# Optimization experiments

Measured on AMD Instinct MI355X. Metric: run time of the kernel, lower is better.

Reference implementation:

```python
import jax, jax.numpy as jnp
import numpy as np

HEADS = 16
KEY_SIZE = 64
SIZE_PER_HEAD = 64
OUT_DIM = HEADS * SIZE_PER_HEAD  # 1024
BIG = 1e10
B, LQ, LK = 2, 2048, 2048


def setup_inputs() -> dict:
    key = jax.random.key(0)
    ks = jax.random.split(key, 8)
    q = jax.random.normal(ks[0], (B, LQ, OUT_DIM), dtype=jnp.float32)
    k = jax.random.normal(ks[1], (B, LK, OUT_DIM), dtype=jnp.float32)
    v = jax.random.normal(ks[2], (B, LK, OUT_DIM), dtype=jnp.float32)
    v_mask = (jax.random.uniform(ks[3], (B, LK)) > 0.1).astype(jnp.float32)
    q_mask = (jax.random.uniform(ks[4], (B, LQ)) > 0.1).astype(jnp.float32)
    # bias-free Linear weights, torch layout [out_features, in_features]
    s = 1.0 / np.sqrt(OUT_DIM)
    Wq = jax.random.normal(ks[5], (HEADS * KEY_SIZE, OUT_DIM), dtype=jnp.float32) * s
    Wk = jax.random.normal(ks[6], (HEADS * KEY_SIZE, OUT_DIM), dtype=jnp.float32) * s
    Wv = jax.random.normal(ks[7], (OUT_DIM, OUT_DIM), dtype=jnp.float32) * s
    return {"q": q, "k": k, "v": v, "v_mask": v_mask, "q_mask": q_mask,
            "Wq": Wq, "Wk": Wk, "Wv": Wv}


def _attention(q, k, v, v_mask, q_mask, Wq, Wk, Wv):
    b, lq, _ = q.shape
    lk = k.shape[1]
    # projections (torch Linear: x @ W.T)
    qw = jnp.einsum('bld,ed->ble', q, Wq).reshape(b, lq, HEADS, KEY_SIZE)
    kw = jnp.einsum('bld,ed->ble', k, Wk).reshape(b, lk, HEADS, KEY_SIZE)
    vw = jnp.einsum('bld,ed->ble', v, Wv).reshape(b, lk, HEADS, SIZE_PER_HEAD)
    # scores [B, H, Lq, Lk]
    a = jnp.einsum('bqhd,bkhd->bhqk', qw, kw) / np.sqrt(KEY_SIZE).astype(np.float32)
    # additive key-padding mask: a - (1 - v_mask) * BIG, broadcast over H and Lq
    a = a - (1.0 - v_mask)[:, None, None, :] * BIG
    # mask_right=True branch: mask = (1 - triu(ones, diag=1)) * BIG, i.e. lower
    # triangle INCLUDING the diagonal is penalized (faithful to source quirk).
    causal = jnp.tril(jnp.ones((lq, lk), dtype=a.dtype)) * BIG  # [Lq, Lk]
    a = a - causal[None, None, :, :]
    a = jax.nn.softmax(a, axis=-1)
    # output [B, Lq, H*dv]
    o = jnp.einsum('bhqk,bkhd->bqhd', a, vw).reshape(b, lq, OUT_DIM)
    o = o * q_mask[:, :, None]
    return o


def reference(q, k, v, v_mask, q_mask, Wq, Wk, Wv):
    return _attention(q, k, v, v_mask, q_mask, Wq, Wk, Wv)
```

## Files before the change

kernel.cpp:

```cpp
#include <hip/hip_runtime.h>
#include <hip/hip_bf16.h>
#include <stdint.h>

#define B_    2
#define SEQ   2048
#define EMB   1024
#define BIGF  1e10f
#define LOG2E 1.4426950408889634f
#define BIG2F (1e10f * LOG2E)
#define C2    (0.125f * LOG2E)

typedef unsigned short u16;
typedef __attribute__((ext_vector_type(4))) u16      u16x4;
typedef __attribute__((ext_vector_type(8))) short    bf8;
typedef __attribute__((ext_vector_type(4))) float    f4;
typedef __attribute__((ext_vector_type(4))) float    fv4;

__device__ inline float bf2f(u16 u){ union{uint32_t i; float f;} v; v.i = ((uint32_t)u) << 16; return v.f; }
__device__ inline u16 f2bf(float f){ union{float f; uint32_t i;} v; v.f = f;
                                     uint32_t r = v.i + 0x7fffu + ((v.i >> 16) & 1u); return (u16)(r >> 16); }
__device__ inline float exp2_hw(float x){ float r; asm("v_exp_f32 %0, %1" : "=v"(r) : "v"(x)); return r; }

__device__ inline void gl_lds16(const void* g, void* l){
  __builtin_amdgcn_global_load_lds((const __attribute__((address_space(1))) uint32_t*)g,
                                   (__attribute__((address_space(3))) uint32_t*)l, 16, 0, 0);
}

struct CvtArgs { const float* src[6]; u16* dst[6]; int n[6]; };

__global__ __launch_bounds__(256) void cvt_bf16(CvtArgs a)
{
  const int seg = blockIdx.y;
  const float* __restrict__ s = a.src[seg];
  u16* __restrict__ d = a.dst[seg];
  const int n = a.n[seg];
  const int i = (blockIdx.x * 256 + threadIdx.x) * 8;
  if (i >= n) return;
  fv4 x0 = *(const fv4*)(s + i);
  fv4 x1 = *(const fv4*)(s + i + 4);
  union { bf8 v; u16 u[8]; } o;
#pragma unroll
  for (int j = 0; j < 4; j++) { o.u[j] = f2bf(x0[j]); o.u[4 + j] = f2bf(x1[j]); }
  *(bf8*)(d + i) = o.v;
}

__global__ __launch_bounds__(256) void proj_gemm(
    const u16* __restrict__ Xq, const u16* __restrict__ Xk, const u16* __restrict__ Xv,
    const u16* __restrict__ Wq, const u16* __restrict__ Wk, const u16* __restrict__ Wv,
    u16* __restrict__ QH, u16* __restrict__ KH, u16* __restrict__ VTB)
{
  __shared__ u16 smem[18432];
  u16* lA = smem;
  u16* lB = smem + 8192;

  const int z = blockIdx.z;
  const u16* X = (z == 0) ? Xq : ((z == 1) ? Xk : Xv);
  const u16* W = (z == 0) ? Wq : ((z == 1) ? Wk : Wv);

  const int tid  = threadIdx.x;
  const int lane = tid & 63;
  const int w    = tid >> 6;
  const int wm   = w >> 1, wn = w & 1;
  const int m0   = blockIdx.x * 128;
  const int n0   = blockIdx.y * 128;
  const int col  = lane & 15, quad = lane >> 4;

  const f4 zero = {0.f, 0.f, 0.f, 0.f};
  f4 acc[4][4];
#pragma unroll
  for (int i = 0; i < 4; i++)
#pragma unroll
    for (int j = 0; j < 4; j++) acc[i][j] = zero;

  for (int k0 = 0; k0 < 1024; k0 += 64) {
    __syncthreads();
#pragma unroll
    for (int j = 0; j < 4; j++) {
      const int kk  = j >> 1;
      const int row = (j & 1) * 64 + w * 16 + (lane >> 2);
      const int cc  = (lane & 3) * 8;
      const size_t g = (size_t)row * 1024 + k0 + kk * 32 + cc;
      gl_lds16(X + (size_t)m0 * 1024 + g, &lA[(j * 256 + w * 64) * 8]);
      gl_lds16(W + (size_t)n0 * 1024 + g, &lB[(j * 256 + w * 64) * 8]);
    }
    __syncthreads();
#pragma unroll
    for (int kk = 0; kk < 2; kk++) {
      const int koff = kk * 4096 + quad * 8;
      bf8 a[4], b[4];
#pragma unroll
      for (int t = 0; t < 4; t++) a[t] = *(const bf8*)&lA[koff + (wm * 64 + t * 16 + col) * 32];
#pragma unroll
      for (int t = 0; t < 4; t++) b[t] = *(const bf8*)&lB[koff + (wn * 64 + t * 16 + col) * 32];
#pragma unroll
      for (int mt = 0; mt < 4; mt++)
#pragma unroll
        for (int nt = 0; nt < 4; nt++)
          acc[mt][nt] = __builtin_amdgcn_mfma_f32_16x16x32_bf16(a[mt], b[nt], acc[mt][nt], 0, 0, 0);
    }
  }

  __syncthreads();
  u16* ep = &smem[w * 4608];

  if (z == 2) {
#pragma unroll
    for (int mt = 0; mt < 4; mt++)
#pragma unroll
      for (int nt = 0; nt < 4; nt++) {
        u16x4 pk = { f2bf(acc[mt][nt][0]), f2bf(acc[mt][nt][1]),
                     f2bf(acc[mt][nt][2]), f2bf(acc[mt][nt][3]) };
        *(u16x4*)&ep[(nt * 16 + col) * 72 + mt * 16 + quad * 4] = pk;
      }
  } else {
#pragma unroll
    for (int mt = 0; mt < 4; mt++)
#pragma unroll
      for (int nt = 0; nt < 4; nt++)
#pragma unroll
        for (int r = 0; r < 4; r++)
          ep[(mt * 16 + quad * 4 + r) * 72 + nt * 16 + col] = f2bf(acc[mt][nt][r]);
  }

  const int bb = m0 >> 11;
  const int h  = (n0 >> 6) + wn;
  const int bh = bb * 16 + h;

  if (z == 0) {
    const int qbase = (m0 & 2047) + wm * 64;
    u16* dst = QH + ((size_t)bh * SEQ + qbase) * 64;
#pragma unroll
    for (int i = 0; i < 8; i++) {
      const int f  = i * 1024 + lane * 16;
      const int ml = i * 8 + (lane >> 3), nl = (lane & 7) * 8;
      *(bf8*)(dst + (f >> 1)) = *(const bf8*)&ep[ml * 72 + nl];
    }
  } else if (z == 1) {
    const int kt = (((m0 & 2047) >> 6) + wm);
    u16* dst = KH + (((size_t)bh * 32 + kt) << 12);
#pragma unroll
    for (int i = 0; i < 8; i++) {
      const int f   = i * 1024 + lane * 16;
      const int dh  = f >> 12;
      const int klc = (f >> 6) & 63;
      const int dlo = (lane & 3) * 8;
      *(bf8*)(dst + (f >> 1)) = *(const bf8*)&ep[klc * 72 + dh * 32 + dlo];
    }
  } else {
    const int kt = (((m0 & 2047) >> 6) + wm);
    u16* dst = VTB + (((size_t)bh * 32 + kt) << 12);
#pragma unroll
    for (int i = 0; i < 8; i++) {
      const int f   = i * 1024 + lane * 16;
      const int kk  = f >> 12;
      const int d   = (f >> 6) & 63;
      const int klo = (lane & 3) * 8;
      *(bf8*)(dst + (f >> 1)) = *(const bf8*)&ep[d * 72 + kk * 32 + klo];
    }
  }
}

__global__ __launch_bounds__(256) void sumv(const u16* __restrict__ VTB,
                                            const float* __restrict__ vmask,
                                            float* __restrict__ fb)
{
  const int w = threadIdx.x >> 6, lane = threadIdx.x & 63;
  const int gw = blockIdx.x * 4 + w;
  const int b = gw >> 10, e = gw & 1023;
  const int h = e >> 6, d = e & 63;
  const int bh = b * 16 + h;
  const float* vm = vmask + b * SEQ;
  float s = 0.f, c = 0.f;
  for (int kt = 0; kt < 32; kt++) {
    const u16 val = VTB[(((size_t)bh * 32 + kt) << 12) + (lane >> 5) * 2048 + d * 32 + (lane & 31)];
    const float m = vm[kt * 64 + lane];
    s += m * bf2f(val); c += m;
  }
#pragma unroll
  for (int o = 1; o < 64; o <<= 1) { s += __shfl_xor(s, o); c += __shfl_xor(c, o); }
  if (lane == 0) fb[gw] = s / c;
}

__global__ __launch_bounds__(256) void attn(
    const u16* __restrict__ QH, const u16* __restrict__ KH, const u16* __restrict__ VTB,
    const float* __restrict__ vmask, const float* __restrict__ qmask,
    const float* __restrict__ fb, float* __restrict__ OUT)
{
  __shared__ float pen[SEQ];
  __shared__ u16   sK[2][4096];
  __shared__ u16   sV[2][4096];
  __shared__ u16   P[4 * 16 * 72];

  const int tid = threadIdx.x, lane = tid & 63, w = tid >> 6;
  const int i   = blockIdx.x;
  const int xcd = i & 7;
  const int j   = i >> 3;
  const int bh  = xcd + 8 * (j >> 4);
  const int qpair = j & 15;
  const int b = bh >> 4, h = bh & 15;
  const int col = lane & 15, quad = lane >> 4;
  const int wb = w * 16 * 72;

  for (int t = tid; t < SEQ; t += 256)
    pen[t] = (1.0f - vmask[b * SEQ + t]) * BIG2F;

  const u16* kbase = KH  + (((size_t)bh * 32) << 12);
  const u16* vbase = VTB + (((size_t)bh * 32) << 12);

  for (int pass = 0; pass < 2; pass++) {
    const int qx = pass ? (31 - qpair) : qpair;
    const int q0 = qx * 64;

    bf8 bQ[2];
#pragma unroll
    for (int dh = 0; dh < 2; dh++)
      bQ[dh] = *(const bf8*)&QH[((size_t)bh * SEQ + q0 + w * 16 + col) * 64 + dh * 32 + quad * 8];

    const f4 zero = {0.f, 0.f, 0.f, 0.f};
    f4 accO[4];
    float l_acc = 0.f;
#pragma unroll
    for (int t = 0; t < 4; t++) accO[t] = zero;

    __syncthreads();
    {
      const size_t toff = ((size_t)qx << 12) + w * 1024 + lane * 8;
      gl_lds16(kbase + toff,       &sK[0][w * 1024]);
      gl_lds16(kbase + toff + 512, &sK[0][w * 1024 + 512]);
      gl_lds16(vbase + toff,       &sV[0][w * 1024]);
      gl_lds16(vbase + toff + 512, &sV[0][w * 1024 + 512]);
    }

    const int ntile = 32 - qx;
    for (int it = 0; it < ntile; it++) {
      __syncthreads();
      if (it + 1 < ntile) {
        const int nb = (it + 1) & 1;
        const size_t toff = ((size_t)(qx + it + 1) << 12) + w * 1024 + lane * 8;
        gl_lds16(kbase + toff,       &sK[nb][w * 1024]);
        gl_lds16(kbase + toff + 512, &sK[nb][w * 1024 + 512]);
        gl_lds16(vbase + toff,       &sV[nb][w * 1024]);
        gl_lds16(vbase + toff + 512, &sV[nb][w * 1024 + 512]);
      }
      const u16* cK = sK[it & 1];
      const u16* cV = sV[it & 1];
      const int k0 = (qx + it) * 64;

      f4 accS[4];
#pragma unroll
      for (int t = 0; t < 4; t++) accS[t] = zero;
#pragma unroll
      for (int nt = 0; nt < 4; nt++)
#pragma unroll
        for (int dh = 0; dh < 2; dh++) {
          bf8 aK = *(const bf8*)&cK[dh * 2048 + (nt * 16 + col) * 32 + quad * 8];
          accS[nt] = __builtin_amdgcn_mfma_f32_16x16x32_bf16(aK, bQ[dh], accS[nt], 0, 0, 0);
        }

      float p[4][4];
      fv4 pv[4];
#pragma unroll
      for (int nt = 0; nt < 4; nt++) pv[nt] = *(const fv4*)&pen[k0 + nt * 16 + quad * 4];
      if (it == 0) {
#pragma unroll
        for (int nt = 0; nt < 4; nt++)
#pragma unroll
          for (int r = 0; r < 4; r++) {
            float sv = fmaf(accS[nt][r], C2, -pv[nt][r]);
            if (nt * 16 + quad * 4 + r <= w * 16 + col) sv -= BIG2F;
            p[nt][r] = exp2_hw(sv);
          }
      } else {
#pragma unroll
        for (int nt = 0; nt < 4; nt++)
#pragma unroll
          for (int r = 0; r < 4; r++)
            p[nt][r] = exp2_hw(fmaf(accS[nt][r], C2, -pv[nt][r]));
      }
#pragma unroll
      for (int nt = 0; nt < 4; nt++)
        l_acc += (p[nt][0] + p[nt][1]) + (p[nt][2] + p[nt][3]);

#pragma unroll
      for (int nt = 0; nt < 4; nt++) {
        union { u16x4 v; u16 u[4]; } pk;
        union { __hip_bfloat162 h2; u16 u[2]; } c0, c1;
        float2 f01; f01.x = p[nt][0]; f01.y = p[nt][1];
        float2 f23; f23.x = p[nt][2]; f23.y = p[nt][3];
        c0.h2 = __float22bfloat162_rn(f01);
        c1.h2 = __float22bfloat162_rn(f23);
        pk.u[0] = c0.u[0]; pk.u[1] = c0.u[1]; pk.u[2] = c1.u[0]; pk.u[3] = c1.u[1];
        *(u16x4*)&P[wb + col * 72 + nt * 16 + quad * 4] = pk.v;
      }

#pragma unroll
      for (int kk = 0; kk < 2; kk++) {
        bf8 bP = *(const bf8*)&P[wb + col * 72 + kk * 32 + quad * 8];
#pragma unroll
        for (int nt = 0; nt < 4; nt++) {
          bf8 aV = *(const bf8*)&cV[kk * 2048 + (nt * 16 + col) * 32 + quad * 8];
          accO[nt] = __builtin_amdgcn_mfma_f32_16x16x32_bf16(aV, bP, accO[nt], 0, 0, 0);
        }
      }
    }

    float l = l_acc;
    l += __shfl_xor(l, 16); l += __shfl_xor(l, 32);
    const int q = q0 + w * 16 + col;
    const float qm = qmask[b * SEQ + q];
    float* op = OUT + (size_t)(b * SEQ + q) * EMB + h * 64;
    if (l == 0.0f) {
#pragma unroll
      for (int nt = 0; nt < 4; nt++) {
        fv4 f = *(const fv4*)&fb[b * 1024 + h * 64 + nt * 16 + quad * 4];
        f *= qm;
        *(fv4*)(op + nt * 16 + quad * 4) = f;
      }
    } else {
      const float s = qm / l;
#pragma unroll
      for (int nt = 0; nt < 4; nt++) {
        fv4 f = { accO[nt][0] * s, accO[nt][1] * s, accO[nt][2] * s, accO[nt][3] * s };
        *(fv4*)(op + nt * 16 + quad * 4) = f;
      }
    }
  }
}

extern "C" void kernel_launch(void* const* d_in, const int* in_sizes, int n_in,
                              void* d_out, int out_size, void* d_ws, size_t ws_size,
                              hipStream_t stream)
{
  const float* q  = (const float*)d_in[0];
  const float* k  = (const float*)d_in[1];
  const float* v  = (const float*)d_in[2];
  const float* vm = (const float*)d_in[3];
  const float* qm = (const float*)d_in[4];
  const float* Wq = (const float*)d_in[5];
  const float* Wk = (const float*)d_in[6];
  const float* Wv = (const float*)d_in[7];
  float* out = (float*)d_out;

  const size_t NBIG = (size_t)B_ * SEQ * EMB;
  const size_t NW   = (size_t)EMB * EMB;

  u16* qb  = (u16*)d_ws;
  u16* kb  = qb  + NBIG;
  u16* vb  = kb  + NBIG;
  u16* Wqb = vb  + NBIG;
  u16* Wkb = Wqb + NW;
  u16* Wvb = Wkb + NW;
  u16* QH  = Wvb + NW;
  u16* KH  = QH  + NBIG;
  u16* VTB = KH  + NBIG;
  float* fb = (float*)(VTB + NBIG);

  CvtArgs ca;
  ca.src[0] = q;  ca.dst[0] = qb;  ca.n[0] = (int)NBIG;
  ca.src[1] = k;  ca.dst[1] = kb;  ca.n[1] = (int)NBIG;
  ca.src[2] = v;  ca.dst[2] = vb;  ca.n[2] = (int)NBIG;
  ca.src[3] = Wq; ca.dst[3] = Wqb; ca.n[3] = (int)NW;
  ca.src[4] = Wk; ca.dst[4] = Wkb; ca.n[4] = (int)NW;
  ca.src[5] = Wv; ca.dst[5] = Wvb; ca.n[5] = (int)NW;

  cvt_bf16<<<dim3((unsigned)(NBIG / 8 / 256), 6, 1), 256, 0, stream>>>(ca);
  proj_gemm<<<dim3(32, 8, 3), 256, 0, stream>>>(qb, kb, vb, Wqb, Wkb, Wvb, QH, KH, VTB);
  sumv<<<dim3(512, 1, 1), 256, 0, stream>>>(VTB, vm, fb);
  attn<<<dim3(512, 1, 1), 256, 0, stream>>>(QH, KH, VTB, vm, qm, fb, out);
}
```

Measured before the change: 199.9 us.

## Restructure attention to 32x32 MFMA with 128-row query tiles and global penalty

The attention kernel now uses 2-wave blocks, each covering 64 query rows with 32x32x16 bf16 MFMAs. Each block handles one 128-query tile (paired in two rounds for causal balance) instead of two 64-row passes. The key-padding penalty is precomputed once in the conversion kernel rather than per block in LDS. The sumv kernel is also rewritten to use vectorized loads with fewer blocks. The aim is to raise MFMA efficiency and K/V reuse per LDS load, at the cost of fewer waves per block and more register pressure.

```diff
diff --git a/kernel.cpp b/kernel.cpp
--- a/kernel.cpp
+++ b/kernel.cpp
@@ -5,16 +5,17 @@
 #define B_    2
 #define SEQ   2048
 #define EMB   1024
-#define BIGF  1e10f
 #define LOG2E 1.4426950408889634f
 #define BIG2F (1e10f * LOG2E)
 #define C2    (0.125f * LOG2E)
+#define PS    72
 
 typedef unsigned short u16;
-typedef __attribute__((ext_vector_type(4))) u16      u16x4;
-typedef __attribute__((ext_vector_type(8))) short    bf8;
-typedef __attribute__((ext_vector_type(4))) float    f4;
-typedef __attribute__((ext_vector_type(4))) float    fv4;
+typedef __attribute__((ext_vector_type(4)))  u16   u16x4;
+typedef __attribute__((ext_vector_type(8)))  short bf8;
+typedef __attribute__((ext_vector_type(4)))  float f4;
+typedef __attribute__((ext_vector_type(16))) float fx16;
+typedef __attribute__((ext_vector_type(4)))  float fv4;
 
 __device__ inline float bf2f(u16 u){ union{uint32_t i; float f;} v; v.i = ((uint32_t)u) << 16; return v.f; }
 __device__ inline u16 f2bf(float f){ union{float f; uint32_t i;} v; v.f = f;
@@ -26,18 +27,27 @@
                                    (__attribute__((address_space(3))) uint32_t*)l, 16, 0, 0);
 }
 
-struct CvtArgs { const float* src[6]; u16* dst[6]; int n[6]; };
+struct CvtArgs { const float* src[7]; u16* dst[7]; int n[7]; };
 
 __global__ __launch_bounds__(256) void cvt_bf16(CvtArgs a)
 {
   const int seg = blockIdx.y;
   const float* __restrict__ s = a.src[seg];
-  u16* __restrict__ d = a.dst[seg];
   const int n = a.n[seg];
   const int i = (blockIdx.x * 256 + threadIdx.x) * 8;
   if (i >= n) return;
   fv4 x0 = *(const fv4*)(s + i);
   fv4 x1 = *(const fv4*)(s + i + 4);
+  if (seg == 6) {
+    float* pd = (float*)a.dst[6];
+    fv4 p0, p1;
+#pragma unroll
+    for (int j = 0; j < 4; j++) { p0[j] = (1.0f - x0[j]) * BIG2F; p1[j] = (1.0f - x1[j]) * BIG2F; }
+    *(fv4*)(pd + i) = p0;
+    *(fv4*)(pd + i + 4) = p1;
+    return;
+  }
+  u16* __restrict__ d = a.dst[seg];
   union { bf8 v; u16 u[8]; } o;
 #pragma unroll
   for (int j = 0; j < 4; j++) { o.u[j] = f2bf(x0[j]); o.u[4 + j] = f2bf(x1[j]); }
@@ -165,164 +175,180 @@
                                             float* __restrict__ fb)
 {
   const int w = threadIdx.x >> 6, lane = threadIdx.x & 63;
-  const int gw = blockIdx.x * 4 + w;
-  const int b = gw >> 10, e = gw & 1023;
-  const int h = e >> 6, d = e & 63;
-  const int bh = b * 16 + h;
+  const int bh = blockIdx.x >> 1, half = blockIdx.x & 1;
+  const int b = bh >> 4, h = bh & 15;
+  const int d = half * 32 + w * 8 + (lane >> 3);
+  const int k4 = (lane & 7) * 4;
+  const u16* tb = VTB + ((size_t)bh << 17);
   const float* vm = vmask + b * SEQ;
   float s = 0.f, c = 0.f;
-  for (int kt = 0; kt < 32; kt++) {
-    const u16 val = VTB[(((size_t)bh * 32 + kt) << 12) + (lane >> 5) * 2048 + d * 32 + (lane & 31)];
-    const float m = vm[kt * 64 + lane];
-    s += m * bf2f(val); c += m;
-  }
-#pragma unroll
-  for (int o = 1; o < 64; o <<= 1) { s += __shfl_xor(s, o); c += __shfl_xor(c, o); }
-  if (lane == 0) fb[gw] = s / c;
-}
-
-__global__ __launch_bounds__(256) void attn(
+  for (int kt = 0; kt < 32; kt++)
+#pragma unroll
+    for (int kk = 0; kk < 2; kk++) {
+      union { u16x4 v; u16 u[4]; } x;
+      x.v = *(const u16x4*)(tb + (kt << 12) + kk * 2048 + d * 32 + k4);
+      fv4 m = *(const fv4*)(vm + kt * 64 + kk * 32 + k4);
+#pragma unroll
+      for (int j = 0; j < 4; j++) { s += m[j] * bf2f(x.u[j]); c += m[j]; }
+    }
+#pragma unroll
+  for (int o = 1; o < 8; o <<= 1) { s += __shfl_xor(s, o); c += __shfl_xor(c, o); }
+  if ((lane & 7) == 0) fb[b * 1024 + h * 64 + d] = s / c;
+}
+
+__global__ __launch_bounds__(128, 2) void attn(
     const u16* __restrict__ QH, const u16* __restrict__ KH, const u16* __restrict__ VTB,
-    const float* __restrict__ vmask, const float* __restrict__ qmask,
+    const float* __restrict__ penG, const float* __restrict__ qmask,
     const float* __restrict__ fb, float* __restrict__ OUT)
 {
-  __shared__ float pen[SEQ];
-  __shared__ u16   sK[2][4096];
-  __shared__ u16   sV[2][4096];
-  __shared__ u16   P[4 * 16 * 72];
-
-  const int tid = threadIdx.x, lane = tid & 63, w = tid >> 6;
-  const int i   = blockIdx.x;
-  const int xcd = i & 7;
-  const int j   = i >> 3;
-  const int bh  = xcd + 8 * (j >> 4);
-  const int qpair = j & 15;
+  __shared__ u16 sK[2][4096];
+  __shared__ u16 sV[2][4096];
+  __shared__ u16 P[2][64 * PS];
+
+  const int tid = threadIdx.x, lane = tid & 63, wq = tid >> 6;
+  const int lm = lane & 31, hi = lane >> 5;
+  const int i  = blockIdx.x;
+  const int lo = i & 255, rnd = i >> 8;
+  const int xcd = lo & 7, g = lo >> 3;
+  const int bh  = xcd + 8 * (g & 3);
+  const int f   = g >> 2;
+  const int qb  = rnd ? (15 - f) : f;
   const int b = bh >> 4, h = bh & 15;
-  const int col = lane & 15, quad = lane >> 4;
-  const int wb = w * 16 * 72;
-
-  for (int t = tid; t < SEQ; t += 256)
-    pen[t] = (1.0f - vmask[b * SEQ + t]) * BIG2F;
-
-  const u16* kbase = KH  + (((size_t)bh * 32) << 12);
-  const u16* vbase = VTB + (((size_t)bh * 32) << 12);
-
-  for (int pass = 0; pass < 2; pass++) {
-    const int qx = pass ? (31 - qpair) : qpair;
-    const int q0 = qx * 64;
-
-    bf8 bQ[2];
-#pragma unroll
-    for (int dh = 0; dh < 2; dh++)
-      bQ[dh] = *(const bf8*)&QH[((size_t)bh * SEQ + q0 + w * 16 + col) * 64 + dh * 32 + quad * 8];
-
-    const f4 zero = {0.f, 0.f, 0.f, 0.f};
-    f4 accO[4];
-    float l_acc = 0.f;
-#pragma unroll
-    for (int t = 0; t < 4; t++) accO[t] = zero;
-
+  const int q0 = qb * 128;
+  const int t0 = 2 * qb, ntile = 32 - t0;
+
+  const u16* kbase = KH  + ((size_t)bh << 17);
+  const u16* vbase = VTB + ((size_t)bh << 17);
+  const float* penB = penG + b * SEQ;
+  u16* Pw = P[wq];
+
+  bf8 bQ[2][4];
+#pragma unroll
+  for (int qt = 0; qt < 2; qt++)
+#pragma unroll
+    for (int kc = 0; kc < 4; kc++)
+      bQ[qt][kc] = *(const bf8*)&QH[((size_t)bh * SEQ + q0 + wq * 64 + qt * 32 + lm) * 64 + kc * 16 + hi * 8];
+
+  fx16 accO[2][2];
+#pragma unroll
+  for (int a = 0; a < 2; a++)
+#pragma unroll
+    for (int c = 0; c < 2; c++)
+#pragma unroll
+      for (int r = 0; r < 16; r++) accO[a][c][r] = 0.f;
+  float l_part[2] = {0.f, 0.f};
+
+  {
+    const size_t so = ((size_t)t0 << 12) + wq * 2048 + lane * 8;
+#pragma unroll
+    for (int s2 = 0; s2 < 4; s2++) {
+      gl_lds16(kbase + so + s2 * 512, &sK[0][wq * 2048 + s2 * 512]);
+      gl_lds16(vbase + so + s2 * 512, &sV[0][wq * 2048 + s2 * 512]);
+    }
+  }
+
+  for (int it = 0; it < ntile; it++) {
     __syncthreads();
-    {
-      const size_t toff = ((size_t)qx << 12) + w * 1024 + lane * 8;
-      gl_lds16(kbase + toff,       &sK[0][w * 1024]);
-      gl_lds16(kbase + toff + 512, &sK[0][w * 1024 + 512]);
-      gl_lds16(vbase + toff,       &sV[0][w * 1024]);
-      gl_lds16(vbase + toff + 512, &sV[0][w * 1024 + 512]);
-    }
-
-    const int ntile = 32 - qx;
-    for (int it = 0; it < ntile; it++) {
-      __syncthreads();
-      if (it + 1 < ntile) {
-        const int nb = (it + 1) & 1;
-        const size_t toff = ((size_t)(qx + it + 1) << 12) + w * 1024 + lane * 8;
-        gl_lds16(kbase + toff,       &sK[nb][w * 1024]);
-        gl_lds16(kbase + toff + 512, &sK[nb][w * 1024 + 512]);
-        gl_lds16(vbase + toff,       &sV[nb][w * 1024]);
-        gl_lds16(vbase + toff + 512, &sV[nb][w * 1024 + 512]);
+    if (it + 1 < ntile) {
+      const int nb = (it + 1) & 1;
+      const size_t so = ((size_t)(t0 + it + 1) << 12) + wq * 2048 + lane * 8;
+#pragma unroll
+      for (int s2 = 0; s2 < 4; s2++) {
+        gl_lds16(kbase + so + s2 * 512, &sK[nb][wq * 2048 + s2 * 512]);
+        gl_lds16(vbase + so + s2 * 512, &sV[nb][wq * 2048 + s2 * 512]);
       }
-      const u16* cK = sK[it & 1];
-      const u16* cV = sV[it & 1];
-      const int k0 = (qx + it) * 64;
-
-      f4 accS[4];
-#pragma unroll
-      for (int t = 0; t < 4; t++) accS[t] = zero;
-#pragma unroll
-      for (int nt = 0; nt < 4; nt++)
-#pragma unroll
-        for (int dh = 0; dh < 2; dh++) {
-          bf8 aK = *(const bf8*)&cK[dh * 2048 + (nt * 16 + col) * 32 + quad * 8];
-          accS[nt] = __builtin_amdgcn_mfma_f32_16x16x32_bf16(aK, bQ[dh], accS[nt], 0, 0, 0);
+    }
+    if (it < wq) continue;
+    const u16* cK = sK[it & 1];
+    const u16* cV = sV[it & 1];
+    const int k0 = (t0 + it) * 64;
+    const bool diag = (it == wq);
+
+#pragma unroll
+    for (int kt2 = 0; kt2 < 2; kt2++) {
+      bf8 aK[4];
+#pragma unroll
+      for (int kc = 0; kc < 4; kc++)
+        aK[kc] = *(const bf8*)&cK[(kc >> 1) * 2048 + (kt2 * 32 + lm) * 32 + (kc & 1) * 16 + hi * 8];
+      fx16 accS[2];
+#pragma unroll
+      for (int qt = 0; qt < 2; qt++) {
+#pragma unroll
+        for (int r = 0; r < 16; r++) accS[qt][r] = 0.f;
+#pragma unroll
+        for (int kc = 0; kc < 4; kc++)
+          accS[qt] = __builtin_amdgcn_mfma_f32_32x32x16_bf16(aK[kc], bQ[qt][kc], accS[qt], 0, 0, 0);
+      }
+      fv4 pv[4];
+#pragma unroll
+      for (int g4 = 0; g4 < 4; g4++)
+        pv[g4] = *(const fv4*)(penB + k0 + kt2 * 32 + g4 * 8 + hi * 4);
+#pragma unroll
+      for (int qt = 0; qt < 2; qt++) {
+        float p[16];
+#pragma unroll
+        for (int r = 0; r < 16; r++) {
+          float sv = fmaf(accS[qt][r], C2, -pv[r >> 2][r & 3]);
+          if (diag) {
+            const int key_in = kt2 * 32 + (r & 3) + 8 * (r >> 2) + 4 * hi;
+            if (key_in <= qt * 32 + lm) sv -= BIG2F;
+          }
+          p[r] = exp2_hw(sv);
+          l_part[qt] += p[r];
         }
-
-      float p[4][4];
-      fv4 pv[4];
-#pragma unroll
-      for (int nt = 0; nt < 4; nt++) pv[nt] = *(const fv4*)&pen[k0 + nt * 16 + quad * 4];
-      if (it == 0) {
-#pragma unroll
-        for (int nt = 0; nt < 4; nt++)
-#pragma unroll
-          for (int r = 0; r < 4; r++) {
-            float sv = fmaf(accS[nt][r], C2, -pv[nt][r]);
-            if (nt * 16 + quad * 4 + r <= w * 16 + col) sv -= BIG2F;
-            p[nt][r] = exp2_hw(sv);
-          }
-      } else {
-#pragma unroll
-        for (int nt = 0; nt < 4; nt++)
-#pragma unroll
-          for (int r = 0; r < 4; r++)
-            p[nt][r] = exp2_hw(fmaf(accS[nt][r], C2, -pv[nt][r]));
-      }
-#pragma unroll
-      for (int nt = 0; nt < 4; nt++)
-        l_acc += (p[nt][0] + p[nt][1]) + (p[nt][2] + p[nt][3]);
-
-#pragma unroll
-      for (int nt = 0; nt < 4; nt++) {
-        union { u16x4 v; u16 u[4]; } pk;
-        union { __hip_bfloat162 h2; u16 u[2]; } c0, c1;
-        float2 f01; f01.x = p[nt][0]; f01.y = p[nt][1];
-        float2 f23; f23.x = p[nt][2]; f23.y = p[nt][3];
-        c0.h2 = __float22bfloat162_rn(f01);
-        c1.h2 = __float22bfloat162_rn(f23);
-        pk.u[0] = c0.u[0]; pk.u[1] = c0.u[1]; pk.u[2] = c1.u[0]; pk.u[3] = c1.u[1];
-        *(u16x4*)&P[wb + col * 72 + nt * 16 + quad * 4] = pk.v;
-      }
-
-#pragma unroll
-      for (int kk = 0; kk < 2; kk++) {
-        bf8 bP = *(const bf8*)&P[wb + col * 72 + kk * 32 + quad * 8];
-#pragma unroll
-        for (int nt = 0; nt < 4; nt++) {
-          bf8 aV = *(const bf8*)&cV[kk * 2048 + (nt * 16 + col) * 32 + quad * 8];
-          accO[nt] = __builtin_amdgcn_mfma_f32_16x16x32_bf16(aV, bP, accO[nt], 0, 0, 0);
+#pragma unroll
+        for (int g4 = 0; g4 < 4; g4++) {
+          u16x4 pk = { f2bf(p[g4 * 4]), f2bf(p[g4 * 4 + 1]), f2bf(p[g4 * 4 + 2]), f2bf(p[g4 * 4 + 3]) };
+          *(u16x4*)&Pw[(qt * 32 + lm) * PS + kt2 * 32 + g4 * 8 + hi * 4] = pk;
         }
       }
     }
 
-    float l = l_acc;
-    l += __shfl_xor(l, 16); l += __shfl_xor(l, 32);
-    const int q = q0 + w * 16 + col;
+    bf8 bP[2][4];
+#pragma unroll
+    for (int qt = 0; qt < 2; qt++)
+#pragma unroll
+      for (int kc = 0; kc < 4; kc++)
+        bP[qt][kc] = *(const bf8*)&Pw[(qt * 32 + lm) * PS + kc * 16 + hi * 8];
+#pragma unroll
+    for (int dt2 = 0; dt2 < 2; dt2++) {
+      bf8 aV[4];
+#pragma unroll
+      for (int kc = 0; kc < 4; kc++)
+        aV[kc] = *(const bf8*)&cV[(kc >> 1) * 2048 + (dt2 * 32 + lm) * 32 + (kc & 1) * 16 + hi * 8];
+#pragma unroll
+      for (int qt = 0; qt < 2; qt++)
+#pragma unroll
+        for (int kc = 0; kc < 4; kc++)
+          accO[dt2][qt] = __builtin_amdgcn_mfma_f32_32x32x16_bf16(aV[kc], bP[qt][kc], accO[dt2][qt], 0, 0, 0);
+    }
+  }
+
+#pragma unroll
+  for (int qt = 0; qt < 2; qt++) {
+    float l = l_part[qt] + __shfl_xor(l_part[qt], 32);
+    const int q = q0 + wq * 64 + qt * 32 + lm;
     const float qm = qmask[b * SEQ + q];
     float* op = OUT + (size_t)(b * SEQ + q) * EMB + h * 64;
     if (l == 0.0f) {
 #pragma unroll
-      for (int nt = 0; nt < 4; nt++) {
-        fv4 f = *(const fv4*)&fb[b * 1024 + h * 64 + nt * 16 + quad * 4];
-        f *= qm;
-        *(fv4*)(op + nt * 16 + quad * 4) = f;
-      }
+      for (int dt2 = 0; dt2 < 2; dt2++)
+#pragma unroll
+        for (int g4 = 0; g4 < 4; g4++) {
+          fv4 fbv = *(const fv4*)&fb[b * 1024 + h * 64 + dt2 * 32 + g4 * 8 + hi * 4];
+          fbv *= qm;
+          *(fv4*)(op + dt2 * 32 + g4 * 8 + hi * 4) = fbv;
+        }
     } else {
-      const float s = qm / l;
-#pragma unroll
-      for (int nt = 0; nt < 4; nt++) {
-        fv4 f = { accO[nt][0] * s, accO[nt][1] * s, accO[nt][2] * s, accO[nt][3] * s };
-        *(fv4*)(op + nt * 16 + quad * 4) = f;
-      }
+      const float sc = qm / l;
+#pragma unroll
+      for (int dt2 = 0; dt2 < 2; dt2++)
+#pragma unroll
+        for (int g4 = 0; g4 < 4; g4++) {
+          fv4 ov = { accO[dt2][qt][g4 * 4] * sc, accO[dt2][qt][g4 * 4 + 1] * sc,
+                     accO[dt2][qt][g4 * 4 + 2] * sc, accO[dt2][qt][g4 * 4 + 3] * sc };
+          *(fv4*)(op + dt2 * 32 + g4 * 8 + hi * 4) = ov;
+        }
     }
   }
 }
@@ -353,18 +379,20 @@
   u16* QH  = Wvb + NW;
   u16* KH  = QH  + NBIG;
   u16* VTB = KH  + NBIG;
-  float* fb = (float*)(VTB + NBIG);
+  float* fb   = (float*)(VTB + NBIG);
+  float* penG = fb + 2048;
 
   CvtArgs ca;
-  ca.src[0] = q;  ca.dst[0] = qb;  ca.n[0] = (int)NBIG;
-  ca.src[1] = k;  ca.dst[1] = kb;  ca.n[1] = (int)NBIG;
-  ca.src[2] = v;  ca.dst[2] = vb;  ca.n[2] = (int)NBIG;
-  ca.src[3] = Wq; ca.dst[3] = Wqb; ca.n[3] = (int)NW;
-  ca.src[4] = Wk; ca.dst[4] = Wkb; ca.n[4] = (int)NW;
-  ca.src[5] = Wv; ca.dst[5] = Wvb; ca.n[5] = (int)NW;
-
-  cvt_bf16<<<dim3((unsigned)(NBIG / 8 / 256), 6, 1), 256, 0, stream>>>(ca);
+  ca.src[0] = q;  ca.dst[0] = qb;          ca.n[0] = (int)NBIG;
+  ca.src[1] = k;  ca.dst[1] = kb;          ca.n[1] = (int)NBIG;
+  ca.src[2] = v;  ca.dst[2] = vb;          ca.n[2] = (int)NBIG;
+  ca.src[3] = Wq; ca.dst[3] = Wqb;         ca.n[3] = (int)NW;
+  ca.src[4] = Wk; ca.dst[4] = Wkb;         ca.n[4] = (int)NW;
+  ca.src[5] = Wv; ca.dst[5] = Wvb;         ca.n[5] = (int)NW;
+  ca.src[6] = vm; ca.dst[6] = (u16*)penG;  ca.n[6] = B_ * SEQ;
+
+  cvt_bf16<<<dim3((unsigned)(NBIG / 8 / 256), 7, 1), 256, 0, stream>>>(ca);
   proj_gemm<<<dim3(32, 8, 3), 256, 0, stream>>>(qb, kb, vb, Wqb, Wkb, Wvb, QH, KH, VTB);
-  sumv<<<dim3(512, 1, 1), 256, 0, stream>>>(VTB, vm, fb);
-  attn<<<dim3(512, 1, 1), 256, 0, stream>>>(QH, KH, VTB, vm, qm, fb, out);
-}
+  sumv<<<dim3(64, 1, 1), 256, 0, stream>>>(VTB, vm, fb);
+  attn<<<dim3(512, 1, 1), 128, 0, stream>>>(QH, KH, VTB, penG, qm, fb, out);
+}
```

Result: slower. 230.6 us (+15.4%).
